# Kernel optimization log

Measured on AMD Instinct MI355X. Metric: run time of the kernel, lower is better.

Reference implementation:

```python
import jax, jax.numpy as jnp
import numpy as np

ANCHORS = [[(0.0156,0.0203),(0.025,0.0469),(0.0516,0.0359)],
           [(0.0469,0.0953),(0.0969,0.0703),(0.0922,0.1859)],
           [(0.1813,0.1406),(0.2438,0.3094),(0.5828,0.5094)]]
IMG = 640.0; NC = 80; NA = 3
LAM_NOOBJ = 1.0; LAM_OBJ = 1.0; LAM_CLS = 1.0; LAM_BOX = 5.0
ALPHA = 0.25; GAMMA = 2.0
GRIDS = [(80, 80), (40, 40), (20, 20)]


def _bce(x, t):
    # numerically-stable BCEWithLogits, reduction='none'
    return jnp.maximum(x, 0.0) - x * t + jnp.log1p(jnp.exp(-jnp.abs(x)))


def _focal(x, t):
    p = jax.nn.sigmoid(x)
    pt = p * t + (1.0 - p) * (1.0 - t)
    at = ALPHA * t + (1.0 - ALPHA) * (1.0 - t)
    return at * (1.0 - pt) ** GAMMA


def setup_inputs() -> dict:
    key = jax.random.key(0)
    ks = jax.random.split(key, 6)
    p0 = jax.random.normal(ks[0], (16, 255, 80, 80), jnp.float32)
    p1 = jax.random.normal(ks[1], (16, 255, 40, 40), jnp.float32)
    p2 = jax.random.normal(ks[2], (16, 255, 20, 20), jnp.float32)
    cxy = jax.random.uniform(ks[3], (16, 32, 2), jnp.float32, 32.0, 608.0)
    wh = jax.random.uniform(ks[4], (16, 32, 2), jnp.float32, 8.0, 256.0)
    target_boxes = jnp.clip(jnp.concatenate([cxy - wh / 2, cxy + wh / 2], -1), 0.0, IMG)
    target_labels = jax.random.randint(ks[5], (16, 32), 0, NC)
    return {"p0": p0, "p1": p1, "p2": p2, "target_boxes": target_boxes, "target_labels": target_labels}


def _loss(preds, boxes, labels):
    anchors = jnp.asarray(ANCHORS, jnp.float32)  # (3, 3, 2)
    B, N = labels.shape
    x1, y1, x2, y2 = boxes[..., 0], boxes[..., 1], boxes[..., 2], boxes[..., 3]
    bw = jnp.clip((x2 - x1) / IMG, 1e-6, 1.0)
    bh = jnp.clip((y2 - y1) / IMG, 1e-6, 1.0)
    # shape IoU against all 9 anchors -> top-1 (scale, anchor) per GT
    aw = anchors.reshape(-1, 2)  # (9, 2)
    inter = jnp.minimum(bw[..., None], aw[:, 0]) * jnp.minimum(bh[..., None], aw[:, 1])
    iou = inter / (bw[..., None] * bh[..., None] + aw[:, 0] * aw[:, 1] - inter + 1e-9)  # (B,N,9)
    best = jnp.argmax(iou, -1)
    scale_idx = best // NA
    anchor_idx = best % NA
    valid = (labels >= 0) & (labels < NC)
    cx = jnp.clip((x1 + x2) * 0.5 / IMG, 0.0, 1.0 - 1e-6)
    cy = jnp.clip((y1 + y2) * 0.5 / IMG, 0.0, 1.0 - 1e-6)
    oh = jax.nn.one_hot(labels, NC, dtype=jnp.float32)  # (B,N,NC)
    tb = jnp.stack([cx, cy, bw, bh], -1)  # (B,N,4) normalized cxcywh
    obj_loss = 0.0; cls_loss = 0.0; box_loss = 0.0; npos = 0.0
    for s, (pred, (h, w)) in enumerate(zip(preds, GRIDS)):
        pred = pred.reshape(B, NA, 5 + NC, h, w)
        gx = cx * w; gy = cy * h
        gi = jnp.clip(jnp.floor(gx), 0, w - 1).astype(jnp.int32)
        gj = jnp.clip(jnp.floor(gy), 0, h - 1).astype(jnp.int32)
        fx = gx - gi; fy = gy - gj
        base = valid & (scale_idx == s)
        ones = jnp.ones_like(fx, bool)
        cand = [(0, 0, ones), (-1, 0, fx < 0.5), (1, 0, fx >= 0.5), (0, -1, fy < 0.5), (0, 1, fy >= 0.5)]
        Ms, GIs, GJs = [], [], []
        for di, dj, keep in cand:
            ngi = gi + di; ngj = gj + dj
            inb = (ngi >= 0) & (ngi < w) & (ngj >= 0) & (ngj < h)
            Ms.append(base & keep & inb)
            GIs.append(jnp.clip(ngi, 0, w - 1))
            GJs.append(jnp.clip(ngj, 0, h - 1))
        M = jnp.stack(Ms); GI = jnp.stack(GIs); GJ = jnp.stack(GJs)  # (5,B,N)
        bidx = jnp.arange(B, dtype=jnp.int32)[None, :, None]
        aidx = jnp.broadcast_to(anchor_idx.astype(jnp.int32)[None], M.shape)
        flat = ((bidx * NA + aidx) * h + GJ) * w + GI  # (5,B,N) index into (B,NA,h,w)
        ncell = B * NA * h * w
        safe = jnp.where(M, flat, ncell)  # invalid -> dummy row
        pos = jax.lax.stop_gradient(
            jnp.zeros(ncell + 1).at[safe].max(M.astype(jnp.float32))[:ncell].reshape(B, NA, h, w))
        cls_t = jax.lax.stop_gradient(
            jnp.zeros((ncell + 1, NC)).at[safe].max(
                jnp.broadcast_to(oh[None], (5, B, N, NC)) * M[..., None].astype(jnp.float32)
            )[:ncell].reshape(B, NA, h, w, NC))
        box_t = jnp.zeros((ncell + 1, 4)).at[safe].set(
            jnp.broadcast_to(tb[None], (5, B, N, 4)))[:ncell].reshape(B, NA, h, w, 4)
        # decode (YOLOv5 parameterization), normalized coords
        sig = jax.nn.sigmoid
        pxy = 2.0 * sig(pred[:, :, :2]) - 0.5  # (B,NA,2,h,w)
        gxr = jnp.arange(w, dtype=jnp.float32)[None, None, None, :]
        gyr = jnp.arange(h, dtype=jnp.float32)[None, None, :, None]
        pcx = (gxr + pxy[:, :, 0]) / w
        pcy = (gyr + pxy[:, :, 1]) / h
        pwh = (2.0 * sig(pred[:, :, 2:4])) ** 2 * anchors[s][None, :, :, None, None]
        pw = pwh[:, :, 0]; ph = pwh[:, :, 1]
        tcx = box_t[..., 0]; tcy = box_t[..., 1]; tw = box_t[..., 2]; th = box_t[..., 3]
        px1, px2 = pcx - pw / 2, pcx + pw / 2; py1, py2 = pcy - ph / 2, pcy + ph / 2
        tx1, tx2 = tcx - tw / 2, tcx + tw / 2; ty1, ty2 = tcy - th / 2, tcy + th / 2
        iw = jnp.maximum(jnp.minimum(px2, tx2) - jnp.maximum(px1, tx1), 0.0)
        ih = jnp.maximum(jnp.minimum(py2, ty2) - jnp.maximum(py1, ty1), 0.0)
        it = iw * ih
        un = pw * ph + tw * th - it + 1e-9
        iouc = it / un
        enc = (jnp.maximum(px2, tx2) - jnp.minimum(px1, tx1)) * (jnp.maximum(py2, ty2) - jnp.minimum(py1, ty1)) + 1e-9
        giou = iouc - (enc - un) / enc
        l1 = jnp.abs(pcx - tcx) + jnp.abs(pcy - tcy) + jnp.abs(pw - tw) + jnp.abs(ph - th)
        box_loss = box_loss + (((1.0 - giou) + l1) * pos).sum()
        pcls = jnp.transpose(pred[:, :, 5:], (0, 1, 3, 4, 2))  # (B,NA,h,w,NC)
        cls_loss = cls_loss + (_bce(pcls, cls_t).sum(-1) * pos).sum()
        pobj = pred[:, :, 4]
        fb = _focal(pobj, pos) * _bce(pobj, pos)
        obj_loss = obj_loss + (fb * jnp.where(pos > 0, LAM_OBJ, LAM_NOOBJ)).mean()
        npos = npos + pos.sum()
    d = jnp.maximum(npos, 1.0)
    return obj_loss + LAM_CLS * cls_loss / d + LAM_BOX * box_loss / d


def reference(p0, p1, p2, target_boxes, target_labels):
    return _loss([p0, p1, p2], target_boxes, target_labels)
```

## Files before the change

kernel.cpp:

```cpp
#include <hip/hip_runtime.h>
#include <math.h>


#define IMGF 640.0f
#define NCLS 80
#define NAK 3
#define NB 16
#define NT 32
#define H0 80
#define H1 40
#define H2 20
#define NCELL0 (NB * NAK * H0 * H0)
#define NCELL1 (NB * NAK * H1 * H1)
#define NCELL2 (NB * NAK * H2 * H2)
#define NCELL_TOTAL (NCELL0 + NCELL1 + NCELL2)
#define MAXPOS (5 * NB * NT)
#define NDENSE (NCELL_TOTAL / 4)
#define NDBLK ((NDENSE + 255) / 256)

__device__ __constant__ float c_anchors[9][2] = {
    {0.0156f, 0.0203f}, {0.025f, 0.0469f}, {0.0516f, 0.0359f},
    {0.0469f, 0.0953f}, {0.0969f, 0.0703f}, {0.0922f, 0.1859f},
    {0.1813f, 0.1406f}, {0.2438f, 0.3094f}, {0.5828f, 0.5094f}};

__device__ inline float sgm(float x) { return 1.f / (1.f + expf(-x)); }
__device__ inline float bcef(float x, float t) {
    return fmaxf(x, 0.f) - x * t + log1pf(expf(-fabsf(x)));
}
__device__ inline float focal_bce(float x, float t) {
    float p = sgm(x);
    float pt = p * t + (1.f - p) * (1.f - t);
    float at = 0.25f * t + 0.75f * (1.f - t);
    float omp = 1.f - pt;
    return at * omp * omp * bcef(x, t);
}

__global__ __launch_bounds__(512) void assign_kernel(
    const float* __restrict__ boxes, const int* __restrict__ labels,
    int* __restrict__ order, unsigned int* __restrict__ tmask,
    int* __restrict__ count, int* __restrict__ list) {
    int t = threadIdx.x;
    if (t >= NB * NT) return;
    int b = t >> 5;
    int n = t & 31;
    int lab = labels[t];
    if (lab < 0 || lab >= NCLS) return;
    float x1 = boxes[4 * t + 0], y1 = boxes[4 * t + 1];
    float x2 = boxes[4 * t + 2], y2 = boxes[4 * t + 3];
    float bw = fminf(fmaxf((x2 - x1) / IMGF, 1e-6f), 1.0f);
    float bh = fminf(fmaxf((y2 - y1) / IMGF, 1e-6f), 1.0f);
    float area = bw * bh;
    float best = -1.0f;
    int bestk = 0;
#pragma unroll
    for (int k = 0; k < 9; k++) {
        float aw = c_anchors[k][0], ah = c_anchors[k][1];
        float inter = fminf(bw, aw) * fminf(bh, ah);
        float iou = inter / (area + aw * ah - inter + 1e-9f);
        if (iou > best) { best = iou; bestk = k; }
    }
    int s = bestk / 3, a = bestk - 3 * s;
    float cx = fminf(fmaxf((x1 + x2) * 0.5f / IMGF, 0.f), 1.f - 1e-6f);
    float cy = fminf(fmaxf((y1 + y2) * 0.5f / IMGF, 0.f), 1.f - 1e-6f);
    int hw = (s == 0) ? H0 : ((s == 1) ? H1 : H2);
    int basecell = (s == 0) ? 0 : ((s == 1) ? NCELL0 : (NCELL0 + NCELL1));
    float gx = cx * (float)hw, gy = cy * (float)hw;
    int gi = min(max((int)floorf(gx), 0), hw - 1);
    int gj = min(max((int)floorf(gy), 0), hw - 1);
    float fx = gx - (float)gi, fy = gy - (float)gj;
    const int dis[5] = {0, -1, 1, 0, 0};
    const int djs[5] = {0, 0, 0, -1, 1};
    bool keep[5];
    keep[0] = true;
    keep[1] = (fx < 0.5f);
    keep[2] = (fx >= 0.5f);
    keep[3] = (fy < 0.5f);
    keep[4] = (fy >= 0.5f);
#pragma unroll
    for (int c = 0; c < 5; c++) {
        if (!keep[c]) continue;
        int ngi = gi + dis[c], ngj = gj + djs[c];
        if (ngi < 0 || ngi >= hw || ngj < 0 || ngj >= hw) continue;
        int cell = basecell + ((b * NAK + a) * hw + ngj) * hw + ngi;
        int old = atomicMax(&order[cell], c * (NB * NT) + t);
        atomicOr(&tmask[cell], 1u << n);
        if (old == -1) {
            int pos = atomicAdd(count, 1);
            list[pos] = cell;
        }
    }
}

template <int HWC>
__device__ inline float obj4(const float* __restrict__ p, uint4 tm, int cis,
                             float inv) {
    int q = cis / HWC;
    int off = cis - q * HWC;
    const float4 v =
        *reinterpret_cast<const float4*>(p + ((size_t)q * 85 + 4) * HWC + off);
    float o = focal_bce(v.x, tm.x ? 1.f : 0.f);
    o += focal_bce(v.y, tm.y ? 1.f : 0.f);
    o += focal_bce(v.z, tm.z ? 1.f : 0.f);
    o += focal_bce(v.w, tm.w ? 1.f : 0.f);
    return o * inv;
}

__global__ __launch_bounds__(256) void dense_kernel(
    const float* __restrict__ p0, const float* __restrict__ p1,
    const float* __restrict__ p2, const uint4* __restrict__ tmask4,
    float* __restrict__ dpart) {
    int i = blockIdx.x * 256 + threadIdx.x;
    float obj = 0.f;
    if (i < NDENSE) {
        uint4 tm = tmask4[i];
        int c4 = i * 4;
        if (c4 < NCELL0)
            obj = obj4<H0 * H0>(p0, tm, c4, 1.f / (float)NCELL0);
        else if (c4 < NCELL0 + NCELL1)
            obj = obj4<H1 * H1>(p1, tm, c4 - NCELL0, 1.f / (float)NCELL1);
        else
            obj = obj4<H2 * H2>(p2, tm, c4 - NCELL0 - NCELL1,
                                1.f / (float)NCELL2);
    }
#pragma unroll
    for (int off = 32; off > 0; off >>= 1) obj += __shfl_down(obj, off, 64);
    __shared__ float red[4];
    if ((threadIdx.x & 63) == 0) red[threadIdx.x >> 6] = obj;
    __syncthreads();
    if (threadIdx.x == 0)
        dpart[blockIdx.x] = red[0] + red[1] + red[2] + red[3];
}

__global__ __launch_bounds__(256) void pos_kernel(
    const float* __restrict__ p0, const float* __restrict__ p1,
    const float* __restrict__ p2, const float* __restrict__ boxes,
    const int* __restrict__ labels, const int* __restrict__ order,
    const unsigned int* __restrict__ tmask, const int* __restrict__ count,
    const int* __restrict__ list, float* __restrict__ ppart) {
    int w = (blockIdx.x * 256 + threadIdx.x) >> 6;
    int lane = threadIdx.x & 63;
    if (w >= *count) return;
    int idx = list[w];
    const float* p;
    int hw, s, base;
    if (idx < NCELL0) {
        p = p0; hw = H0; s = 0; base = 0;
    } else if (idx < NCELL0 + NCELL1) {
        p = p1; hw = H1; s = 1; base = NCELL0;
    } else {
        p = p2; hw = H2; s = 2; base = NCELL0 + NCELL1;
    }
    int cell = idx - base;
    int x = cell % hw;
    int r = cell / hw;
    int y = r % hw;
    r /= hw;
    int a = r % NAK;
    int b = r / NAK;
    size_t HW = (size_t)hw * hw;
    const float* pc = p + (size_t)(b * 255 + a * 85) * HW + (size_t)y * hw + x;
    unsigned tm = tmask[idx];
    float cl = 0.f;
#pragma unroll
    for (int rep = 0; rep < 2; rep++) {
        int c = lane + 64 * rep;
        if (c < NCLS) {
            float tt = 0.f;
            unsigned tmp = tm;
            while (tmp) {
                int n = __ffs(tmp) - 1;
                tmp &= tmp - 1;
                if (labels[(b << 5) + n] == c) tt = 1.f;
            }
            cl += bcef(pc[(size_t)(5 + c) * HW], tt);
        }
    }
#pragma unroll
    for (int off = 32; off > 0; off >>= 1) cl += __shfl_down(cl, off, 64);
    if (lane == 0) {
        int wn = order[idx] & (NB * NT - 1);
        float bx1 = boxes[4 * wn + 0], by1 = boxes[4 * wn + 1];
        float bx2 = boxes[4 * wn + 2], by2 = boxes[4 * wn + 3];
        float tw = fminf(fmaxf((bx2 - bx1) / IMGF, 1e-6f), 1.f);
        float th = fminf(fmaxf((by2 - by1) / IMGF, 1e-6f), 1.f);
        float tcx = fminf(fmaxf((bx1 + bx2) * 0.5f / IMGF, 0.f), 1.f - 1e-6f);
        float tcy = fminf(fmaxf((by1 + by2) * 0.5f / IMGF, 0.f), 1.f - 1e-6f);
        float l0 = pc[0], l1 = pc[HW], l2 = pc[2 * HW], l3 = pc[3 * HW];
        float pcx = ((float)x + 2.f * sgm(l0) - 0.5f) / (float)hw;
        float pcy = ((float)y + 2.f * sgm(l1) - 0.5f) / (float)hw;
        float sw = 2.f * sgm(l2), sh = 2.f * sgm(l3);
        float pw = sw * sw * c_anchors[s * 3 + a][0];
        float ph = sh * sh * c_anchors[s * 3 + a][1];
        float px1 = pcx - pw * 0.5f, px2 = pcx + pw * 0.5f;
        float py1 = pcy - ph * 0.5f, py2 = pcy + ph * 0.5f;
        float tx1 = tcx - tw * 0.5f, tx2 = tcx + tw * 0.5f;
        float ty1 = tcy - th * 0.5f, ty2 = tcy + th * 0.5f;
        float iw = fmaxf(fminf(px2, tx2) - fmaxf(px1, tx1), 0.f);
        float ih = fmaxf(fminf(py2, ty2) - fmaxf(py1, ty1), 0.f);
        float it = iw * ih;
        float un = pw * ph + tw * th - it + 1e-9f;
        float iou = it / un;
        float enc = (fmaxf(px2, tx2) - fminf(px1, tx1)) *
                        (fmaxf(py2, ty2) - fminf(py1, ty1)) +
                    1e-9f;
        float giou = iou - (enc - un) / enc;
        float l1l = fabsf(pcx - tcx) + fabsf(pcy - tcy) + fabsf(pw - tw) +
                    fabsf(ph - th);
        ppart[2 * w] = cl;
        ppart[2 * w + 1] = 1.f - giou + l1l;
    }
}

__global__ __launch_bounds__(256) void finalize_kernel(
    const float* __restrict__ dpart, const float* __restrict__ ppart,
    const int* __restrict__ count, float* __restrict__ out) {
    int cnt = *count;
    float obj = 0.f, cls = 0.f, box = 0.f;
    for (int i = threadIdx.x; i < NDBLK; i += 256) obj += dpart[i];
    for (int i = threadIdx.x; i < cnt; i += 256) {
        cls += ppart[2 * i];
        box += ppart[2 * i + 1];
    }
#pragma unroll
    for (int off = 32; off > 0; off >>= 1) {
        obj += __shfl_down(obj, off, 64);
        cls += __shfl_down(cls, off, 64);
        box += __shfl_down(box, off, 64);
    }
    __shared__ float red[4][3];
    int wv = threadIdx.x >> 6;
    if ((threadIdx.x & 63) == 0) {
        red[wv][0] = obj;
        red[wv][1] = cls;
        red[wv][2] = box;
    }
    __syncthreads();
    if (threadIdx.x == 0) {
        float o = red[0][0] + red[1][0] + red[2][0] + red[3][0];
        float c = red[0][1] + red[1][1] + red[2][1] + red[3][1];
        float bx = red[0][2] + red[1][2] + red[2][2] + red[3][2];
        float d = fmaxf((float)cnt, 1.f);
        out[0] = o + (c + 5.f * bx) / d;
    }
}

extern "C" void kernel_launch(void* const* d_in, const int* in_sizes, int n_in,
                              void* d_out, int out_size, void* d_ws,
                              size_t ws_size, hipStream_t stream) {
    const float* p0 = (const float*)d_in[0];
    const float* p1 = (const float*)d_in[1];
    const float* p2 = (const float*)d_in[2];
    const float* boxes = (const float*)d_in[3];
    const int* labels = (const int*)d_in[4];
    float* out = (float*)d_out;

    char* ws = (char*)d_ws;
    int* order = (int*)ws;
    size_t off = (size_t)NCELL_TOTAL * 4;
    unsigned int* tmask = (unsigned int*)(ws + off);
    off += (size_t)NCELL_TOTAL * 4;
    int* count = (int*)(ws + off);
    off += 16;
    int* list = (int*)(ws + off);
    off += (size_t)MAXPOS * 4;
    float* dpart = (float*)(ws + off);
    off += (size_t)((NDBLK + 3) / 4 * 4) * 4;
    float* ppart = (float*)(ws + off);

    hipMemsetAsync(order, 0xFF, (size_t)NCELL_TOTAL * 4, stream);
    hipMemsetAsync(tmask, 0, (size_t)NCELL_TOTAL * 4 + 16, stream);

    assign_kernel<<<1, 512, 0, stream>>>(boxes, labels, order, tmask, count,
                                         list);
    dense_kernel<<<NDBLK, 256, 0, stream>>>(p0, p1, p2, (const uint4*)tmask,
                                            dpart);
    pos_kernel<<<(MAXPOS * 64 + 255) / 256, 256, 0, stream>>>(
        p0, p1, p2, boxes, labels, order, tmask, count, list, ppart);
    finalize_kernel<<<1, 256, 0, stream>>>(dpart, ppart, count, out);
}
```

Baseline: 34.70 us.

## Replace global assignment grids with shared-memory hash table and fuse finalize

```diff
diff --git a/kernel.cpp b/kernel.cpp
--- a/kernel.cpp
+++ b/kernel.cpp
@@ -14,9 +14,11 @@
 #define NCELL1 (NB * NAK * H1 * H1)
 #define NCELL2 (NB * NAK * H2 * H2)
 #define NCELL_TOTAL (NCELL0 + NCELL1 + NCELL2)
-#define MAXPOS (5 * NB * NT)
+#define MAXPOS 1536
 #define NDENSE (NCELL_TOTAL / 4)
 #define NDBLK ((NDENSE + 255) / 256)
+#define POS_BLOCKS (MAXPOS * 64 / 256)
+#define HSIZE 4096
 
 __device__ __constant__ float c_anchors[9][2] = {
     {0.0156f, 0.0203f}, {0.025f, 0.0469f}, {0.0516f, 0.0359f},
@@ -37,90 +39,109 @@
 
 __global__ __launch_bounds__(512) void assign_kernel(
     const float* __restrict__ boxes, const int* __restrict__ labels,
-    int* __restrict__ order, unsigned int* __restrict__ tmask,
-    int* __restrict__ count, int* __restrict__ list) {
+    int4* __restrict__ list, int* __restrict__ countg, int* __restrict__ done) {
+    __shared__ int hkey[HSIZE];
+    __shared__ int hord[HSIZE];
+    __shared__ unsigned htm[HSIZE];
+    __shared__ int lcount;
+    for (int i = threadIdx.x; i < HSIZE; i += 512) {
+        hkey[i] = -1;
+        hord[i] = -1;
+        htm[i] = 0u;
+    }
+    if (threadIdx.x == 0) lcount = 0;
+    __syncthreads();
+
     int t = threadIdx.x;
-    if (t >= NB * NT) return;
     int b = t >> 5;
     int n = t & 31;
     int lab = labels[t];
-    if (lab < 0 || lab >= NCLS) return;
-    float x1 = boxes[4 * t + 0], y1 = boxes[4 * t + 1];
-    float x2 = boxes[4 * t + 2], y2 = boxes[4 * t + 3];
-    float bw = fminf(fmaxf((x2 - x1) / IMGF, 1e-6f), 1.0f);
-    float bh = fminf(fmaxf((y2 - y1) / IMGF, 1e-6f), 1.0f);
-    float area = bw * bh;
-    float best = -1.0f;
-    int bestk = 0;
-#pragma unroll
-    for (int k = 0; k < 9; k++) {
-        float aw = c_anchors[k][0], ah = c_anchors[k][1];
-        float inter = fminf(bw, aw) * fminf(bh, ah);
-        float iou = inter / (area + aw * ah - inter + 1e-9f);
-        if (iou > best) { best = iou; bestk = k; }
-    }
-    int s = bestk / 3, a = bestk - 3 * s;
-    float cx = fminf(fmaxf((x1 + x2) * 0.5f / IMGF, 0.f), 1.f - 1e-6f);
-    float cy = fminf(fmaxf((y1 + y2) * 0.5f / IMGF, 0.f), 1.f - 1e-6f);
-    int hw = (s == 0) ? H0 : ((s == 1) ? H1 : H2);
-    int basecell = (s == 0) ? 0 : ((s == 1) ? NCELL0 : (NCELL0 + NCELL1));
-    float gx = cx * (float)hw, gy = cy * (float)hw;
-    int gi = min(max((int)floorf(gx), 0), hw - 1);
-    int gj = min(max((int)floorf(gy), 0), hw - 1);
-    float fx = gx - (float)gi, fy = gy - (float)gj;
-    const int dis[5] = {0, -1, 1, 0, 0};
-    const int djs[5] = {0, 0, 0, -1, 1};
-    bool keep[5];
-    keep[0] = true;
-    keep[1] = (fx < 0.5f);
-    keep[2] = (fx >= 0.5f);
-    keep[3] = (fy < 0.5f);
-    keep[4] = (fy >= 0.5f);
-#pragma unroll
-    for (int c = 0; c < 5; c++) {
-        if (!keep[c]) continue;
-        int ngi = gi + dis[c], ngj = gj + djs[c];
-        if (ngi < 0 || ngi >= hw || ngj < 0 || ngj >= hw) continue;
-        int cell = basecell + ((b * NAK + a) * hw + ngj) * hw + ngi;
-        int old = atomicMax(&order[cell], c * (NB * NT) + t);
-        atomicOr(&tmask[cell], 1u << n);
-        if (old == -1) {
-            int pos = atomicAdd(count, 1);
-            list[pos] = cell;
-        }
+    if (lab >= 0 && lab < NCLS) {
+        float x1 = boxes[4 * t + 0], y1 = boxes[4 * t + 1];
+        float x2 = boxes[4 * t + 2], y2 = boxes[4 * t + 3];
+        float bw = fminf(fmaxf((x2 - x1) / IMGF, 1e-6f), 1.0f);
+        float bh = fminf(fmaxf((y2 - y1) / IMGF, 1e-6f), 1.0f);
+        float area = bw * bh;
+        float best = -1.0f;
+        int bestk = 0;
+#pragma unroll
+        for (int k = 0; k < 9; k++) {
+            float aw = c_anchors[k][0], ah = c_anchors[k][1];
+            float inter = fminf(bw, aw) * fminf(bh, ah);
+            float iou = inter / (area + aw * ah - inter + 1e-9f);
+            if (iou > best) { best = iou; bestk = k; }
+        }
+        int s = bestk / 3, a = bestk - 3 * s;
+        float cx = fminf(fmaxf((x1 + x2) * 0.5f / IMGF, 0.f), 1.f - 1e-6f);
+        float cy = fminf(fmaxf((y1 + y2) * 0.5f / IMGF, 0.f), 1.f - 1e-6f);
+        int hw = (s == 0) ? H0 : ((s == 1) ? H1 : H2);
+        int basecell = (s == 0) ? 0 : ((s == 1) ? NCELL0 : (NCELL0 + NCELL1));
+        float gx = cx * (float)hw, gy = cy * (float)hw;
+        int gi = min(max((int)floorf(gx), 0), hw - 1);
+        int gj = min(max((int)floorf(gy), 0), hw - 1);
+        float fx = gx - (float)gi, fy = gy - (float)gj;
+        const int dis[5] = {0, -1, 1, 0, 0};
+        const int djs[5] = {0, 0, 0, -1, 1};
+        bool keep[5];
+        keep[0] = true;
+        keep[1] = (fx < 0.5f);
+        keep[2] = (fx >= 0.5f);
+        keep[3] = (fy < 0.5f);
+        keep[4] = (fy >= 0.5f);
+#pragma unroll
+        for (int c = 0; c < 5; c++) {
+            if (!keep[c]) continue;
+            int ngi = gi + dis[c], ngj = gj + djs[c];
+            if (ngi < 0 || ngi >= hw || ngj < 0 || ngj >= hw) continue;
+            int cell = basecell + ((b * NAK + a) * hw + ngj) * hw + ngi;
+            unsigned h = ((unsigned)cell * 2654435761u) >> 20;
+            while (true) {
+                int old = atomicCAS(&hkey[h], -1, cell);
+                if (old == -1 || old == cell) break;
+                h = (h + 1) & (HSIZE - 1);
+            }
+            atomicMax(&hord[h], c * (NB * NT) + t);
+            atomicOr(&htm[h], 1u << n);
+        }
+    }
+    __syncthreads();
+    for (int i = threadIdx.x; i < HSIZE; i += 512) {
+        if (hkey[i] >= 0) {
+            int p = atomicAdd(&lcount, 1);
+            list[p] = make_int4(hkey[i], hord[i], (int)htm[i], 0);
+        }
+    }
+    __syncthreads();
+    if (threadIdx.x == 0) {
+        *countg = lcount;
+        *done = 0;
     }
 }
 
 template <int HWC>
-__device__ inline float obj4(const float* __restrict__ p, uint4 tm, int cis,
-                             float inv) {
+__device__ inline float obj4(const float* __restrict__ p, int cis, float inv) {
     int q = cis / HWC;
     int off = cis - q * HWC;
     const float4 v =
         *reinterpret_cast<const float4*>(p + ((size_t)q * 85 + 4) * HWC + off);
-    float o = focal_bce(v.x, tm.x ? 1.f : 0.f);
-    o += focal_bce(v.y, tm.y ? 1.f : 0.f);
-    o += focal_bce(v.z, tm.z ? 1.f : 0.f);
-    o += focal_bce(v.w, tm.w ? 1.f : 0.f);
-    return o * inv;
+    return (focal_bce(v.x, 0.f) + focal_bce(v.y, 0.f) + focal_bce(v.z, 0.f) +
+            focal_bce(v.w, 0.f)) *
+           inv;
 }
 
 __global__ __launch_bounds__(256) void dense_kernel(
     const float* __restrict__ p0, const float* __restrict__ p1,
-    const float* __restrict__ p2, const uint4* __restrict__ tmask4,
-    float* __restrict__ dpart) {
+    const float* __restrict__ p2, float* __restrict__ dpart) {
     int i = blockIdx.x * 256 + threadIdx.x;
     float obj = 0.f;
     if (i < NDENSE) {
-        uint4 tm = tmask4[i];
         int c4 = i * 4;
         if (c4 < NCELL0)
-            obj = obj4<H0 * H0>(p0, tm, c4, 1.f / (float)NCELL0);
+            obj = obj4<H0 * H0>(p0, c4, 1.f / (float)NCELL0);
         else if (c4 < NCELL0 + NCELL1)
-            obj = obj4<H1 * H1>(p1, tm, c4 - NCELL0, 1.f / (float)NCELL1);
+            obj = obj4<H1 * H1>(p1, c4 - NCELL0, 1.f / (float)NCELL1);
         else
-            obj = obj4<H2 * H2>(p2, tm, c4 - NCELL0 - NCELL1,
-                                1.f / (float)NCELL2);
+            obj = obj4<H2 * H2>(p2, c4 - NCELL0 - NCELL1, 1.f / (float)NCELL2);
     }
 #pragma unroll
     for (int off = 32; off > 0; off >>= 1) obj += __shfl_down(obj, off, 64);
@@ -134,113 +155,131 @@
 __global__ __launch_bounds__(256) void pos_kernel(
     const float* __restrict__ p0, const float* __restrict__ p1,
     const float* __restrict__ p2, const float* __restrict__ boxes,
-    const int* __restrict__ labels, const int* __restrict__ order,
-    const unsigned int* __restrict__ tmask, const int* __restrict__ count,
-    const int* __restrict__ list, float* __restrict__ ppart) {
+    const int* __restrict__ labels, const int4* __restrict__ list,
+    const int* __restrict__ countg, int* __restrict__ done,
+    const float* __restrict__ dpart, float* __restrict__ ppart,
+    float* __restrict__ out) {
+    int cnt = *countg;
     int w = (blockIdx.x * 256 + threadIdx.x) >> 6;
     int lane = threadIdx.x & 63;
-    if (w >= *count) return;
-    int idx = list[w];
-    const float* p;
-    int hw, s, base;
-    if (idx < NCELL0) {
-        p = p0; hw = H0; s = 0; base = 0;
-    } else if (idx < NCELL0 + NCELL1) {
-        p = p1; hw = H1; s = 1; base = NCELL0;
-    } else {
-        p = p2; hw = H2; s = 2; base = NCELL0 + NCELL1;
-    }
-    int cell = idx - base;
-    int x = cell % hw;
-    int r = cell / hw;
-    int y = r % hw;
-    r /= hw;
-    int a = r % NAK;
-    int b = r / NAK;
-    size_t HW = (size_t)hw * hw;
-    const float* pc = p + (size_t)(b * 255 + a * 85) * HW + (size_t)y * hw + x;
-    unsigned tm = tmask[idx];
-    float cl = 0.f;
-#pragma unroll
-    for (int rep = 0; rep < 2; rep++) {
-        int c = lane + 64 * rep;
-        if (c < NCLS) {
-            float tt = 0.f;
-            unsigned tmp = tm;
-            while (tmp) {
-                int n = __ffs(tmp) - 1;
-                tmp &= tmp - 1;
-                if (labels[(b << 5) + n] == c) tt = 1.f;
+    if (w < cnt) {
+        int4 rec = list[w];
+        int idx = rec.x;
+        unsigned tm = (unsigned)rec.z;
+        const float* p;
+        int hw, s, base;
+        float inv;
+        if (idx < NCELL0) {
+            p = p0; hw = H0; s = 0; base = 0; inv = 1.f / (float)NCELL0;
+        } else if (idx < NCELL0 + NCELL1) {
+            p = p1; hw = H1; s = 1; base = NCELL0; inv = 1.f / (float)NCELL1;
+        } else {
+            p = p2; hw = H2; s = 2; base = NCELL0 + NCELL1;
+            inv = 1.f / (float)NCELL2;
+        }
+        int cell = idx - base;
+        int x = cell % hw;
+        int r = cell / hw;
+        int y = r % hw;
+        r /= hw;
+        int a = r % NAK;
+        int b = r / NAK;
+        size_t HW = (size_t)hw * hw;
+        const float* pc =
+            p + (size_t)(b * 255 + a * 85) * HW + (size_t)y * hw + x;
+        float cl = 0.f;
+#pragma unroll
+        for (int rep = 0; rep < 2; rep++) {
+            int c = lane + 64 * rep;
+            if (c < NCLS) {
+                float tt = 0.f;
+                unsigned tmp = tm;
+                while (tmp) {
+                    int n = __ffs(tmp) - 1;
+                    tmp &= tmp - 1;
+                    if (labels[(b << 5) + n] == c) tt = 1.f;
+                }
+                cl += bcef(pc[(size_t)(5 + c) * HW], tt);
             }
-            cl += bcef(pc[(size_t)(5 + c) * HW], tt);
-        }
-    }
-#pragma unroll
-    for (int off = 32; off > 0; off >>= 1) cl += __shfl_down(cl, off, 64);
-    if (lane == 0) {
-        int wn = order[idx] & (NB * NT - 1);
-        float bx1 = boxes[4 * wn + 0], by1 = boxes[4 * wn + 1];
-        float bx2 = boxes[4 * wn + 2], by2 = boxes[4 * wn + 3];
-        float tw = fminf(fmaxf((bx2 - bx1) / IMGF, 1e-6f), 1.f);
-        float th = fminf(fmaxf((by2 - by1) / IMGF, 1e-6f), 1.f);
-        float tcx = fminf(fmaxf((bx1 + bx2) * 0.5f / IMGF, 0.f), 1.f - 1e-6f);
-        float tcy = fminf(fmaxf((by1 + by2) * 0.5f / IMGF, 0.f), 1.f - 1e-6f);
-        float l0 = pc[0], l1 = pc[HW], l2 = pc[2 * HW], l3 = pc[3 * HW];
-        float pcx = ((float)x + 2.f * sgm(l0) - 0.5f) / (float)hw;
-        float pcy = ((float)y + 2.f * sgm(l1) - 0.5f) / (float)hw;
-        float sw = 2.f * sgm(l2), sh = 2.f * sgm(l3);
-        float pw = sw * sw * c_anchors[s * 3 + a][0];
-        float ph = sh * sh * c_anchors[s * 3 + a][1];
-        float px1 = pcx - pw * 0.5f, px2 = pcx + pw * 0.5f;
-        float py1 = pcy - ph * 0.5f, py2 = pcy + ph * 0.5f;
-        float tx1 = tcx - tw * 0.5f, tx2 = tcx + tw * 0.5f;
-        float ty1 = tcy - th * 0.5f, ty2 = tcy + th * 0.5f;
-        float iw = fmaxf(fminf(px2, tx2) - fmaxf(px1, tx1), 0.f);
-        float ih = fmaxf(fminf(py2, ty2) - fmaxf(py1, ty1), 0.f);
-        float it = iw * ih;
-        float un = pw * ph + tw * th - it + 1e-9f;
-        float iou = it / un;
-        float enc = (fmaxf(px2, tx2) - fminf(px1, tx1)) *
-                        (fmaxf(py2, ty2) - fminf(py1, ty1)) +
-                    1e-9f;
-        float giou = iou - (enc - un) / enc;
-        float l1l = fabsf(pcx - tcx) + fabsf(pcy - tcy) + fabsf(pw - tw) +
-                    fabsf(ph - th);
-        ppart[2 * w] = cl;
-        ppart[2 * w + 1] = 1.f - giou + l1l;
-    }
-}
-
-__global__ __launch_bounds__(256) void finalize_kernel(
-    const float* __restrict__ dpart, const float* __restrict__ ppart,
-    const int* __restrict__ count, float* __restrict__ out) {
-    int cnt = *count;
-    float obj = 0.f, cls = 0.f, box = 0.f;
-    for (int i = threadIdx.x; i < NDBLK; i += 256) obj += dpart[i];
-    for (int i = threadIdx.x; i < cnt; i += 256) {
-        cls += ppart[2 * i];
-        box += ppart[2 * i + 1];
-    }
-#pragma unroll
-    for (int off = 32; off > 0; off >>= 1) {
-        obj += __shfl_down(obj, off, 64);
-        cls += __shfl_down(cls, off, 64);
-        box += __shfl_down(box, off, 64);
-    }
-    __shared__ float red[4][3];
-    int wv = threadIdx.x >> 6;
-    if ((threadIdx.x & 63) == 0) {
-        red[wv][0] = obj;
-        red[wv][1] = cls;
-        red[wv][2] = box;
-    }
+        }
+#pragma unroll
+        for (int off = 32; off > 0; off >>= 1) cl += __shfl_down(cl, off, 64);
+        if (lane == 0) {
+            float pobj = pc[4 * HW];
+            float objc = (focal_bce(pobj, 1.f) - focal_bce(pobj, 0.f)) * inv;
+            int wn = rec.y & (NB * NT - 1);
+            float bx1 = boxes[4 * wn + 0], by1 = boxes[4 * wn + 1];
+            float bx2 = boxes[4 * wn + 2], by2 = boxes[4 * wn + 3];
+            float tw = fminf(fmaxf((bx2 - bx1) / IMGF, 1e-6f), 1.f);
+            float th = fminf(fmaxf((by2 - by1) / IMGF, 1e-6f), 1.f);
+            float tcx =
+                fminf(fmaxf((bx1 + bx2) * 0.5f / IMGF, 0.f), 1.f - 1e-6f);
+            float tcy =
+                fminf(fmaxf((by1 + by2) * 0.5f / IMGF, 0.f), 1.f - 1e-6f);
+            float l0 = pc[0], l1 = pc[HW], l2 = pc[2 * HW], l3 = pc[3 * HW];
+            float pcx = ((float)x + 2.f * sgm(l0) - 0.5f) / (float)hw;
+            float pcy = ((float)y + 2.f * sgm(l1) - 0.5f) / (float)hw;
+            float sw = 2.f * sgm(l2), sh = 2.f * sgm(l3);
+            float pw = sw * sw * c_anchors[s * 3 + a][0];
+            float ph = sh * sh * c_anchors[s * 3 + a][1];
+            float px1 = pcx - pw * 0.5f, px2 = pcx + pw * 0.5f;
+            float py1 = pcy - ph * 0.5f, py2 = pcy + ph * 0.5f;
+            float tx1 = tcx - tw * 0.5f, tx2 = tcx + tw * 0.5f;
+            float ty1 = tcy - th * 0.5f, ty2 = tcy + th * 0.5f;
+            float iw = fmaxf(fminf(px2, tx2) - fmaxf(px1, tx1), 0.f);
+            float ih = fmaxf(fminf(py2, ty2) - fmaxf(py1, ty1), 0.f);
+            float it = iw * ih;
+            float un = pw * ph + tw * th - it + 1e-9f;
+            float iou = it / un;
+            float enc = (fmaxf(px2, tx2) - fminf(px1, tx1)) *
+                            (fmaxf(py2, ty2) - fminf(py1, ty1)) +
+                        1e-9f;
+            float giou = iou - (enc - un) / enc;
+            float l1l = fabsf(pcx - tcx) + fabsf(pcy - tcy) + fabsf(pw - tw) +
+                        fabsf(ph - th);
+            ppart[3 * w] = cl;
+            ppart[3 * w + 1] = 1.f - giou + l1l;
+            ppart[3 * w + 2] = objc;
+        }
+    }
+    __shared__ int amLast;
     __syncthreads();
     if (threadIdx.x == 0) {
-        float o = red[0][0] + red[1][0] + red[2][0] + red[3][0];
-        float c = red[0][1] + red[1][1] + red[2][1] + red[3][1];
-        float bx = red[0][2] + red[1][2] + red[2][2] + red[3][2];
-        float d = fmaxf((float)cnt, 1.f);
-        out[0] = o + (c + 5.f * bx) / d;
+        __threadfence();
+        int old = atomicAdd(done, 1);
+        amLast = (old == POS_BLOCKS - 1) ? 1 : 0;
+    }
+    __syncthreads();
+    if (amLast) {
+        __threadfence();
+        float obj = 0.f, cls = 0.f, box = 0.f;
+        for (int i = threadIdx.x; i < NDBLK; i += 256) obj += dpart[i];
+        for (int i = threadIdx.x; i < cnt; i += 256) {
+            cls += ppart[3 * i];
+            box += ppart[3 * i + 1];
+            obj += ppart[3 * i + 2];
+        }
+#pragma unroll
+        for (int off = 32; off > 0; off >>= 1) {
+            obj += __shfl_down(obj, off, 64);
+            cls += __shfl_down(cls, off, 64);
+            box += __shfl_down(box, off, 64);
+        }
+        __shared__ float red[4][3];
+        int wv = threadIdx.x >> 6;
+        if ((threadIdx.x & 63) == 0) {
+            red[wv][0] = obj;
+            red[wv][1] = cls;
+            red[wv][2] = box;
+        }
+        __syncthreads();
+        if (threadIdx.x == 0) {
+            float o = red[0][0] + red[1][0] + red[2][0] + red[3][0];
+            float c = red[0][1] + red[1][1] + red[2][1] + red[3][1];
+            float bx = red[0][2] + red[1][2] + red[2][2] + red[3][2];
+            float d = fmaxf((float)cnt, 1.f);
+            out[0] = o + (c + 5.f * bx) / d;
+        }
     }
 }
 
@@ -255,26 +294,17 @@
     float* out = (float*)d_out;
 
     char* ws = (char*)d_ws;
-    int* order = (int*)ws;
-    size_t off = (size_t)NCELL_TOTAL * 4;
-    unsigned int* tmask = (unsigned int*)(ws + off);
-    off += (size_t)NCELL_TOTAL * 4;
-    int* count = (int*)(ws + off);
+    int4* list = (int4*)ws;
+    size_t off = (size_t)MAXPOS * 16;
+    int* countg = (int*)(ws + off);
+    int* done = (int*)(ws + off + 4);
     off += 16;
-    int* list = (int*)(ws + off);
-    off += (size_t)MAXPOS * 4;
     float* dpart = (float*)(ws + off);
     off += (size_t)((NDBLK + 3) / 4 * 4) * 4;
     float* ppart = (float*)(ws + off);
 
-    hipMemsetAsync(order, 0xFF, (size_t)NCELL_TOTAL * 4, stream);
-    hipMemsetAsync(tmask, 0, (size_t)NCELL_TOTAL * 4 + 16, stream);
-
-    assign_kernel<<<1, 512, 0, stream>>>(boxes, labels, order, tmask, count,
-                                         list);
-    dense_kernel<<<NDBLK, 256, 0, stream>>>(p0, p1, p2, (const uint4*)tmask,
-                                            dpart);
-    pos_kernel<<<(MAXPOS * 64 + 255) / 256, 256, 0, stream>>>(
-        p0, p1, p2, boxes, labels, order, tmask, count, list, ppart);
-    finalize_kernel<<<1, 256, 0, stream>>>(dpart, ppart, count, out);
-}
+    assign_kernel<<<1, 512, 0, stream>>>(boxes, labels, list, countg, done);
+    dense_kernel<<<NDBLK, 256, 0, stream>>>(p0, p1, p2, dpart);
+    pos_kernel<<<POS_BLOCKS, 256, 0, stream>>>(p0, p1, p2, boxes, labels, list,
+                                               countg, done, dpart, ppart, out);
+}
```

Result: faster. 31.19 us (-10.1%).
